# Kernel optimization log

Measured on AMD Instinct MI355X. Metric: run time of the kernel, lower is better.

## Reference

```python
import math
import jax, jax.numpy as jnp
import numpy as np

K_MODES = 8
L_ITERS = 8
ALPHA_INIT = 2000.0
TAU_INIT = 0.01


def setup_inputs() -> dict:
    key = jax.random.key(0)
    B, T, C = 64, 4096, 16
    x = jax.random.normal(key, (B, T, C), dtype=jnp.float32)
    log_alpha = jnp.full((L_ITERS, K_MODES), math.log(ALPHA_INIT), dtype=jnp.float32)
    raw_tau = jnp.full((L_ITERS,), math.log(math.expm1(TAU_INIT) + 1e-08), dtype=jnp.float32)
    omega_init = np.linspace(0.05, 0.45, K_MODES)
    raw_omega = jnp.asarray(np.log(2.0 * omega_init / (1.0 - 2.0 * omega_init + 1e-08)), dtype=jnp.float32)
    return {"x": x, "log_alpha": log_alpha, "raw_tau": raw_tau, "raw_omega": raw_omega}


def reference(x, log_alpha, raw_tau, raw_omega):
    B, T, C = x.shape
    L, K = log_alpha.shape
    T_rfft = T // 2 + 1

    alpha = jnp.exp(log_alpha)                    # (L, K)
    tau = jax.nn.softplus(raw_tau)                # (L,)
    omega = jax.nn.sigmoid(raw_omega) * 0.5       # (K,)

    freqs = jnp.linspace(0.0, 0.5, T_rfft, dtype=x.dtype)  # (T_rfft,)
    # (B, T, C) -> (B*C, T)
    x_bc = jnp.transpose(x, (0, 2, 1)).reshape(B * C, T)
    f_hat = jnp.fft.rfft(x_bc, axis=-1)           # (B*C, T_rfft) complex

    # Precompute all denominators: (L, K, T_rfft)
    denom = 1.0 + 2.0 * alpha[:, :, None] * (freqs[None, None, :] - omega[None, :, None]) ** 2

    u0 = jnp.zeros((B * C, K, T_rfft), dtype=f_hat.dtype)
    lam0 = jnp.zeros_like(f_hat)

    def step(carry, per_layer):
        u, lam = carry
        den_l, tau_l = per_layer
        u_sum = u.sum(axis=1)  # (B*C, T_rfft)
        # Jacobi update for all K modes simultaneously
        numerator = f_hat[:, None, :] - (u_sum[:, None, :] - u) + 0.5 * lam[:, None, :]
        u_new = numerator / den_l[None, :, :]
        lam_new = lam + tau_l * (f_hat - u_new.sum(axis=1))
        return (u_new, lam_new), None

    (u_final, _), _ = jax.lax.scan(step, (u0, lam0), (denom, tau))

    modes_flat = jnp.fft.irfft(u_final, n=T, axis=-1)  # (B*C, K, T)
    modes = jnp.transpose(modes_flat.reshape(B, C, K, T), (0, 2, 3, 1))  # (B, K, T, C)
    return modes
```

## Files before the change

kernel.cpp:

```cpp
#include <hip/hip_runtime.h>
#include <math.h>

#ifndef M_PI
#define M_PI 3.14159265358979323846
#endif

#define T_LEN 4096
#define M_LEN 2048
#define NFREQ 2049
#define KM 8
#define LI 8
#define CD 16

template <int NT>
__device__ __forceinline__ float2* fft2048(float2* a, float2* b, int tid, float sign) {
    float2* src = a;
    float2* dst = b;
    int l = 1024;
    #pragma unroll 1
    for (int s = 0; s < 11; ++s) {
        float piol = sign * (float)M_PI / (float)l;
        #pragma unroll
        for (int ii = 0; ii < 1024 / NT; ++ii) {
            int i = tid + ii * NT;
            int j = i >> s;
            float2 A = src[i];
            float2 B = src[i + 1024];
            float ang = piol * (float)j;
            float sw, cw;
            __sincosf(ang, &sw, &cw);
            float2 sum = make_float2(A.x + B.x, A.y + B.y);
            float2 dif = make_float2(A.x - B.x, A.y - B.y);
            float2 tw = make_float2(dif.x * cw - dif.y * sw, dif.x * sw + dif.y * cw);
            int p = i + (j << s);
            dst[p] = sum;
            dst[p + (1 << s)] = tw;
        }
        __syncthreads();
        float2* t = src; src = dst; dst = t;
        l >>= 1;
    }
    return src;
}

__global__ void __launch_bounds__(512)
k_fwd_iter(const float* __restrict__ x,
           const float* __restrict__ log_alpha,
           const float* __restrict__ raw_tau,
           const float* __restrict__ raw_omega,
           float2* __restrict__ u_ws)
{
    __shared__ float2 bufA[M_LEN];
    __shared__ float2 bufB[M_LEN];
    __shared__ float s_2a[LI * KM];
    __shared__ float s_tau[LI];
    __shared__ float s_om[KM];

    const int tid = threadIdx.x;
    const int row = blockIdx.x;
    const int b = row >> 4;
    const int c = row & 15;

    if (tid < LI * KM) s_2a[tid] = 2.0f * __expf(log_alpha[tid]);
    if (tid < LI)      s_tau[tid] = log1pf(__expf(raw_tau[tid]));
    if (tid < KM)      s_om[tid]  = 0.5f / (1.0f + __expf(-raw_omega[tid]));

    const float* xr = x + (size_t)b * T_LEN * CD + c;
    #pragma unroll
    for (int q = 0; q < 4; ++q) {
        int n = tid + q * 512;
        float e = xr[(size_t)(2 * n) * CD];
        float o = xr[(size_t)(2 * n + 1) * CD];
        bufA[n] = make_float2(e, o);
    }
    __syncthreads();

    float2* Z = fft2048<512>(bufA, bufB, tid, -1.0f);

    const size_t sb = (size_t)(b * (KM * CD) + c);

    for (int f = tid; f < NFREQ; f += 512) {
        float2 Zk = Z[f & (M_LEN - 1)];
        float2 Zm = Z[(M_LEN - f) & (M_LEN - 1)];
        float2 E = make_float2(0.5f * (Zk.x + Zm.x), 0.5f * (Zk.y - Zm.y));
        float2 D = make_float2(0.5f * (Zk.x - Zm.x), 0.5f * (Zk.y + Zm.y));
        float2 O = make_float2(D.y, -D.x);
        float ang = -2.0f * (float)M_PI * (float)f / (float)T_LEN;
        float sw, cw;
        __sincosf(ang, &sw, &cw);
        float fhx = E.x + cw * O.x - sw * O.y;
        float fhy = E.y + cw * O.y + sw * O.x;

        float freq = (float)f * (0.5f / (float)M_LEN);
        float dd[KM];
        #pragma unroll
        for (int k = 0; k < KM; ++k) {
            float d = freq - s_om[k];
            dd[k] = d * d;
        }

        float2 u[KM];
        #pragma unroll
        for (int k = 0; k < KM; ++k) u[k] = make_float2(0.f, 0.f);
        float lamx = 0.f, lamy = 0.f;

        #pragma unroll
        for (int l = 0; l < LI; ++l) {
            float usx = 0.f, usy = 0.f;
            #pragma unroll
            for (int k = 0; k < KM; ++k) { usx += u[k].x; usy += u[k].y; }
            float bx = fhx - usx + 0.5f * lamx;
            float by = fhy - usy + 0.5f * lamy;
            float sx = 0.f, sy = 0.f;
            #pragma unroll
            for (int k = 0; k < KM; ++k) {
                float den = fmaf(s_2a[l * KM + k], dd[k], 1.0f);
                float r = __builtin_amdgcn_rcpf(den);
                float ux = (bx + u[k].x) * r;
                float uy = (by + u[k].y) * r;
                u[k].x = ux; u[k].y = uy;
                sx += ux; sy += uy;
            }
            lamx += s_tau[l] * (fhx - sx);
            lamy += s_tau[l] * (fhy - sy);
        }

        #pragma unroll
        for (int k = 0; k < KM; ++k) {
            u_ws[(sb + (size_t)k * CD) * NFREQ + f] = u[k];
        }
    }
}

__global__ void __launch_bounds__(1024)
k_inv(const float2* __restrict__ u_ws, float* __restrict__ out)
{
    __shared__ float2 bufA[NFREQ];
    __shared__ float2 bufB[M_LEN];
    const int tid = threadIdx.x;
    const int bk = blockIdx.x;

    float val[CD][4];

    #pragma unroll
    for (int c = 0; c < CD; ++c) {
        const float2* sp = u_ws + (size_t)(bk * CD + c) * NFREQ;
        bufA[tid] = sp[tid];
        bufA[tid + 1024] = sp[tid + 1024];
        if (tid == 0) bufA[2048] = sp[2048];
        __syncthreads();

        #pragma unroll
        for (int jj = 0; jj < 2; ++jj) {
            int j = tid + jj * 1024;
            float2 Xj = bufA[j];
            float2 Xm = bufA[M_LEN - j];
            float2 E = make_float2(0.5f * (Xj.x + Xm.x), 0.5f * (Xj.y - Xm.y));
            float2 D = make_float2(0.5f * (Xj.x - Xm.x), 0.5f * (Xj.y + Xm.y));
            float ang = 2.0f * (float)M_PI * (float)j / (float)T_LEN;
            float sw, cw;
            __sincosf(ang, &sw, &cw);
            float2 O = make_float2(cw * D.x - sw * D.y, cw * D.y + sw * D.x);
            const float sc = 1.0f / (float)M_LEN;
            bufB[j] = make_float2((E.x - O.y) * sc, (E.y + O.x) * sc);
        }
        __syncthreads();

        float2* res = fft2048<1024>(bufB, bufA, tid, 1.0f);
        float2 z0 = res[2 * tid];
        float2 z1 = res[2 * tid + 1];
        val[c][0] = z0.x;
        val[c][1] = z0.y;
        val[c][2] = z1.x;
        val[c][3] = z1.y;
        __syncthreads();
    }

    float4* op = (float4*)(out + ((size_t)bk * T_LEN + (size_t)(4 * tid)) * CD);
    #pragma unroll
    for (int r = 0; r < 4; ++r) {
        #pragma unroll
        for (int g = 0; g < 4; ++g) {
            op[r * 4 + g] = make_float4(val[4 * g + 0][r], val[4 * g + 1][r],
                                        val[4 * g + 2][r], val[4 * g + 3][r]);
        }
    }
}

extern "C" void kernel_launch(void* const* d_in, const int* in_sizes, int n_in,
                              void* d_out, int out_size, void* d_ws, size_t ws_size,
                              hipStream_t stream) {
    const float* x         = (const float*)d_in[0];
    const float* log_alpha = (const float*)d_in[1];
    const float* raw_tau   = (const float*)d_in[2];
    const float* raw_omega = (const float*)d_in[3];
    float* out = (float*)d_out;
    float2* u_ws = (float2*)d_ws;

    k_fwd_iter<<<dim3(64 * CD), dim3(512), 0, stream>>>(x, log_alpha, raw_tau,
                                                        raw_omega, u_ws);
    k_inv<<<dim3(64 * KM), dim3(1024), 0, stream>>>(u_ws, out);
}
```

Measured before the change: 396.8 us.

## Process two channels per inverse-FFT pass and load spectrum directly from global

Measured after the change: 374.3 us. 1.06x faster.

```diff
diff --git a/kernel.cpp b/kernel.cpp
--- a/kernel.cpp
+++ b/kernel.cpp
@@ -135,45 +135,89 @@
 __global__ void __launch_bounds__(1024)
 k_inv(const float2* __restrict__ u_ws, float* __restrict__ out)
 {
-    __shared__ float2 bufA[NFREQ];
-    __shared__ float2 bufB[M_LEN];
+    __shared__ __align__(16) float2 buf[2][2][M_LEN];
+
     const int tid = threadIdx.x;
     const int bk = blockIdx.x;
 
     float val[CD][4];
-
-    #pragma unroll
-    for (int c = 0; c < CD; ++c) {
-        const float2* sp = u_ws + (size_t)(bk * CD + c) * NFREQ;
-        bufA[tid] = sp[tid];
-        bufA[tid + 1024] = sp[tid + 1024];
-        if (tid == 0) bufA[2048] = sp[2048];
-        __syncthreads();
-
-        #pragma unroll
-        for (int jj = 0; jj < 2; ++jj) {
-            int j = tid + jj * 1024;
-            float2 Xj = bufA[j];
-            float2 Xm = bufA[M_LEN - j];
-            float2 E = make_float2(0.5f * (Xj.x + Xm.x), 0.5f * (Xj.y - Xm.y));
-            float2 D = make_float2(0.5f * (Xj.x - Xm.x), 0.5f * (Xj.y + Xm.y));
-            float ang = 2.0f * (float)M_PI * (float)j / (float)T_LEN;
+    const float sc = 1.0f / (float)M_LEN;
+
+    #pragma unroll 1
+    for (int cp = 0; cp < 8; ++cp) {
+        if (cp > 0) {
+            #pragma unroll
+            for (int ch = 0; ch < 2; ++ch) {
+                int c = 2 * (cp - 1) + ch;
+                float4 z = *(const float4*)&buf[ch][1][2 * tid];
+                val[c][0] = z.x; val[c][1] = z.y; val[c][2] = z.z; val[c][3] = z.w;
+            }
+        }
+
+        #pragma unroll
+        for (int ch = 0; ch < 2; ++ch) {
+            int c = 2 * cp + ch;
+            const float2* sp = u_ws + (size_t)(bk * CD + c) * NFREQ;
+            int j = tid;
+            float2 Xj = sp[j];
+            float2 Xm = sp[M_LEN - j];
+            float Ex = 0.5f * (Xj.x + Xm.x), Ey = 0.5f * (Xj.y - Xm.y);
+            float Dx = 0.5f * (Xj.x - Xm.x), Dy = 0.5f * (Xj.y + Xm.y);
+            float ang = (2.0f * (float)M_PI / (float)T_LEN) * (float)j;
             float sw, cw;
             __sincosf(ang, &sw, &cw);
-            float2 O = make_float2(cw * D.x - sw * D.y, cw * D.y + sw * D.x);
-            const float sc = 1.0f / (float)M_LEN;
-            bufB[j] = make_float2((E.x - O.y) * sc, (E.y + O.x) * sc);
+            float Ox = cw * Dx - sw * Dy;
+            float Oy = cw * Dy + sw * Dx;
+            buf[ch][0][j] = make_float2((Ex - Oy) * sc, (Ey + Ox) * sc);
+            if (j > 0) {
+                buf[ch][0][M_LEN - j] = make_float2((Ex + Oy) * sc, (Ox - Ey) * sc);
+            } else {
+                float2 Xq = sp[1024];
+                buf[ch][0][1024] = make_float2(Xq.x * sc, -Xq.y * sc);
+            }
         }
         __syncthreads();
 
-        float2* res = fft2048<1024>(bufB, bufA, tid, 1.0f);
-        float2 z0 = res[2 * tid];
-        float2 z1 = res[2 * tid + 1];
-        val[c][0] = z0.x;
-        val[c][1] = z0.y;
-        val[c][2] = z1.x;
-        val[c][3] = z1.y;
-        __syncthreads();
+        float2* s0 = buf[0][0]; float2* d0 = buf[0][1];
+        float2* s1 = buf[1][0]; float2* d1 = buf[1][1];
+        #pragma unroll 1
+        for (int s = 0; s < 11; ++s) {
+            const int i = tid;
+            const int j = i >> s;
+            const int m = 1 << s;
+            const int p = i + (j << s);
+            float ang = ((float)M_PI / 1024.0f) * (float)(j << s);
+            float sw, cw;
+            __sincosf(ang, &sw, &cw);
+            {
+                float2 A = s0[i], B = s0[i + 1024];
+                float2 sum = make_float2(A.x + B.x, A.y + B.y);
+                float2 dif = make_float2(A.x - B.x, A.y - B.y);
+                float2 t = make_float2(dif.x * cw - dif.y * sw,
+                                       dif.x * sw + dif.y * cw);
+                d0[p] = sum;
+                d0[p + m] = t;
+            }
+            {
+                float2 A = s1[i], B = s1[i + 1024];
+                float2 sum = make_float2(A.x + B.x, A.y + B.y);
+                float2 dif = make_float2(A.x - B.x, A.y - B.y);
+                float2 t = make_float2(dif.x * cw - dif.y * sw,
+                                       dif.x * sw + dif.y * cw);
+                d1[p] = sum;
+                d1[p + m] = t;
+            }
+            __syncthreads();
+            float2* t0 = s0; s0 = d0; d0 = t0;
+            float2* t1 = s1; s1 = d1; d1 = t1;
+        }
+    }
+
+    #pragma unroll
+    for (int ch = 0; ch < 2; ++ch) {
+        int c = 14 + ch;
+        float4 z = *(const float4*)&buf[ch][1][2 * tid];
+        val[c][0] = z.x; val[c][1] = z.y; val[c][2] = z.z; val[c][3] = z.w;
     }
 
     float4* op = (float4*)(out + ((size_t)bk * T_LEN + (size_t)(4 * tid)) * CD);
```

## Rewrite inverse FFT as in-place radix-8 Stockham with four channels per block

Applied to the files above, without the earlier changes.

New measurement: 414.8 us. +4.5%, slower.

```diff
diff --git a/kernel.cpp b/kernel.cpp
--- a/kernel.cpp
+++ b/kernel.cpp
@@ -11,6 +11,71 @@
 #define KM 8
 #define LI 8
 #define CD 16
+
+__device__ __forceinline__ float2 cadd(float2 a, float2 b){ return make_float2(a.x+b.x, a.y+b.y); }
+__device__ __forceinline__ float2 csub(float2 a, float2 b){ return make_float2(a.x-b.x, a.y-b.y); }
+__device__ __forceinline__ float2 cmul(float2 a, float2 b){ return make_float2(a.x*b.x - a.y*b.y, a.x*b.y + a.y*b.x); }
+__device__ __forceinline__ float2 muli(float2 a){ return make_float2(-a.y, a.x); }
+#define RC 0.70710678118654752440f
+__device__ __forceinline__ float2 mulw81(float2 a){ return make_float2(RC*(a.x-a.y), RC*(a.x+a.y)); }
+__device__ __forceinline__ float2 mulw83(float2 a){ return make_float2(-RC*(a.x+a.y), RC*(a.x-a.y)); }
+
+#define SWZ(i) ((i) ^ (((i) >> 4) & 15))
+
+__device__ __forceinline__ void dft8_inv(const float2 a[8], float2 x[8]) {
+    float2 s0=cadd(a[0],a[4]), s1=cadd(a[1],a[5]), s2=cadd(a[2],a[6]), s3=cadd(a[3],a[7]);
+    float2 d0=csub(a[0],a[4]), d1=csub(a[1],a[5]), d2=csub(a[2],a[6]), d3=csub(a[3],a[7]);
+    d1 = mulw81(d1); d2 = muli(d2); d3 = mulw83(d3);
+    float2 e0=cadd(s0,s2), e2=csub(s0,s2), e1=cadd(s1,s3), e3=muli(csub(s1,s3));
+    float2 f0=cadd(d0,d2), f2=csub(d0,d2), f1=cadd(d1,d3), f3=muli(csub(d1,d3));
+    x[0]=cadd(e0,e1); x[4]=csub(e0,e1); x[2]=cadd(e2,e3); x[6]=csub(e2,e3);
+    x[1]=cadd(f0,f1); x[5]=csub(f0,f1); x[3]=cadd(f2,f3); x[7]=csub(f2,f3);
+}
+
+template<int MSTAGE>
+__device__ __forceinline__ void r8_stage(float2* S, int lt) {
+    float2 a[8];
+    #pragma unroll
+    for (int k = 0; k < 8; ++k) a[k] = S[SWZ(lt + 256*k)];
+    __syncthreads();
+    float2 x[8];
+    dft8_inv(a, x);
+    const int j = lt / MSTAGE;
+    const int r = lt % MSTAGE;
+    float th = ((float)M_PI / 1024.0f) * (float)(j * MSTAGE);
+    float swv, cwv; __sincosf(th, &swv, &cwv);
+    float2 w1 = make_float2(cwv, swv);
+    float2 w2 = cmul(w1,w1), w3 = cmul(w2,w1), w4 = cmul(w2,w2);
+    float2 w5 = cmul(w3,w2), w6 = cmul(w3,w3), w7 = cmul(w4,w3);
+    x[1]=cmul(x[1],w1); x[2]=cmul(x[2],w2); x[3]=cmul(x[3],w3);
+    x[4]=cmul(x[4],w4); x[5]=cmul(x[5],w5); x[6]=cmul(x[6],w6); x[7]=cmul(x[7],w7);
+    const int base = r + 8*MSTAGE*j;
+    #pragma unroll
+    for (int k = 0; k < 8; ++k) S[SWZ(base + MSTAGE*k)] = x[k];
+    __syncthreads();
+}
+
+__device__ __forceinline__ void r4_stage_pair(float2* S, int lt) {
+    float2 b[2][4];
+    #pragma unroll
+    for (int h = 0; h < 2; ++h) {
+        int i2 = lt + 256*h;
+        #pragma unroll
+        for (int k = 0; k < 4; ++k) b[h][k] = S[SWZ(i2 + 512*k)];
+    }
+    __syncthreads();
+    #pragma unroll
+    for (int h = 0; h < 2; ++h) {
+        int i2 = lt + 256*h;
+        float2 s02=cadd(b[h][0],b[h][2]), d02=csub(b[h][0],b[h][2]);
+        float2 s13=cadd(b[h][1],b[h][3]), d13=muli(csub(b[h][1],b[h][3]));
+        S[SWZ(i2 +    0)] = cadd(s02,s13);
+        S[SWZ(i2 +  512)] = cadd(d02,d13);
+        S[SWZ(i2 + 1024)] = csub(s02,s13);
+        S[SWZ(i2 + 1536)] = csub(d02,d13);
+    }
+    __syncthreads();
+}
 
 template <int NT>
 __device__ __forceinline__ float2* fft2048(float2* a, float2* b, int tid, float sign) {
@@ -135,54 +200,67 @@
 __global__ void __launch_bounds__(1024)
 k_inv(const float2* __restrict__ u_ws, float* __restrict__ out)
 {
-    __shared__ float2 bufA[NFREQ];
-    __shared__ float2 bufB[M_LEN];
+    __shared__ float2 S[4][M_LEN];
+
     const int tid = threadIdx.x;
-    const int bk = blockIdx.x;
+    const int g   = tid >> 8;
+    const int lt  = tid & 255;
+    const int bk  = blockIdx.x;
 
     float val[CD][4];
-
-    #pragma unroll
-    for (int c = 0; c < CD; ++c) {
-        const float2* sp = u_ws + (size_t)(bk * CD + c) * NFREQ;
-        bufA[tid] = sp[tid];
-        bufA[tid + 1024] = sp[tid + 1024];
-        if (tid == 0) bufA[2048] = sp[2048];
+    const float sc = 1.0f / (float)M_LEN;
+
+    #pragma unroll
+    for (int cp = 0; cp < 4; ++cp) {
+        const int c0 = 4 * cp;
+        const float2* sp = u_ws + (size_t)(bk * CD + c0 + g) * NFREQ;
+
+        #pragma unroll
+        for (int q = 0; q < 4; ++q) {
+            int j = lt + 256 * q;
+            float2 Xj = sp[j];
+            float2 Xm = sp[M_LEN - j];
+            float Ex = 0.5f * (Xj.x + Xm.x), Ey = 0.5f * (Xj.y - Xm.y);
+            float Dx = 0.5f * (Xj.x - Xm.x), Dy = 0.5f * (Xj.y + Xm.y);
+            float ang = (2.0f * (float)M_PI / (float)T_LEN) * (float)j;
+            float swv, cwv;
+            __sincosf(ang, &swv, &cwv);
+            float Ox = cwv * Dx - swv * Dy;
+            float Oy = cwv * Dy + swv * Dx;
+            S[g][SWZ(j)] = make_float2((Ex - Oy) * sc, (Ey + Ox) * sc);
+            if (j > 0) {
+                S[g][SWZ(M_LEN - j)] = make_float2((Ex + Oy) * sc, (Ox - Ey) * sc);
+            } else {
+                float2 Xq = sp[1024];
+                S[g][SWZ(1024)] = make_float2(Xq.x * sc, -Xq.y * sc);
+            }
+        }
         __syncthreads();
 
-        #pragma unroll
-        for (int jj = 0; jj < 2; ++jj) {
-            int j = tid + jj * 1024;
-            float2 Xj = bufA[j];
-            float2 Xm = bufA[M_LEN - j];
-            float2 E = make_float2(0.5f * (Xj.x + Xm.x), 0.5f * (Xj.y - Xm.y));
-            float2 D = make_float2(0.5f * (Xj.x - Xm.x), 0.5f * (Xj.y + Xm.y));
-            float ang = 2.0f * (float)M_PI * (float)j / (float)T_LEN;
-            float sw, cw;
-            __sincosf(ang, &sw, &cw);
-            float2 O = make_float2(cw * D.x - sw * D.y, cw * D.y + sw * D.x);
-            const float sc = 1.0f / (float)M_LEN;
-            bufB[j] = make_float2((E.x - O.y) * sc, (E.y + O.x) * sc);
+        r8_stage<1>(S[g], lt);
+        r8_stage<8>(S[g], lt);
+        r8_stage<64>(S[g], lt);
+        r4_stage_pair(S[g], lt);
+
+        #pragma unroll
+        for (int cc = 0; cc < 4; ++cc) {
+            float2 z0 = S[cc][SWZ(2 * tid)];
+            float2 z1 = S[cc][SWZ(2 * tid + 1)];
+            val[c0 + cc][0] = z0.x;
+            val[c0 + cc][1] = z0.y;
+            val[c0 + cc][2] = z1.x;
+            val[c0 + cc][3] = z1.y;
         }
         __syncthreads();
-
-        float2* res = fft2048<1024>(bufB, bufA, tid, 1.0f);
-        float2 z0 = res[2 * tid];
-        float2 z1 = res[2 * tid + 1];
-        val[c][0] = z0.x;
-        val[c][1] = z0.y;
-        val[c][2] = z1.x;
-        val[c][3] = z1.y;
-        __syncthreads();
     }
 
     float4* op = (float4*)(out + ((size_t)bk * T_LEN + (size_t)(4 * tid)) * CD);
     #pragma unroll
     for (int r = 0; r < 4; ++r) {
         #pragma unroll
-        for (int g = 0; g < 4; ++g) {
-            op[r * 4 + g] = make_float4(val[4 * g + 0][r], val[4 * g + 1][r],
-                                        val[4 * g + 2][r], val[4 * g + 3][r]);
+        for (int g2 = 0; g2 < 4; ++g2) {
+            op[r * 4 + g2] = make_float4(val[4 * g2 + 0][r], val[4 * g2 + 1][r],
+                                         val[4 * g2 + 2][r], val[4 * g2 + 3][r]);
         }
     }
 }
```

## Use radix-8 in-place FFT with swizzled LDS in forward kernel, two rows per block

Applied to the files above, without the earlier changes.

New measurement: 393.9 us. Within noise of the previous version (-0.7%).

```diff
diff --git a/kernel.cpp b/kernel.cpp
--- a/kernel.cpp
+++ b/kernel.cpp
@@ -11,6 +11,88 @@
 #define KM 8
 #define LI 8
 #define CD 16
+
+__device__ __forceinline__ float2 cadd(float2 a, float2 b){ return make_float2(a.x+b.x, a.y+b.y); }
+__device__ __forceinline__ float2 csub(float2 a, float2 b){ return make_float2(a.x-b.x, a.y-b.y); }
+__device__ __forceinline__ float2 cmul(float2 a, float2 b){ return make_float2(a.x*b.x - a.y*b.y, a.x*b.y + a.y*b.x); }
+#define RC 0.70710678118654752440f
+
+template<int SGN>
+__device__ __forceinline__ float2 muli_s(float2 a){
+    return (SGN > 0) ? make_float2(-a.y, a.x) : make_float2(a.y, -a.x);
+}
+template<int SGN>
+__device__ __forceinline__ float2 w81_s(float2 a){
+    return (SGN > 0) ? make_float2(RC*(a.x-a.y), RC*(a.x+a.y))
+                     : make_float2(RC*(a.x+a.y), RC*(a.y-a.x));
+}
+template<int SGN>
+__device__ __forceinline__ float2 w83_s(float2 a){
+    return (SGN > 0) ? make_float2(-RC*(a.x+a.y), RC*(a.x-a.y))
+                     : make_float2(RC*(a.y-a.x), -RC*(a.x+a.y));
+}
+
+#define SWZ(i) ((i) ^ (((i) >> 4) & 15))
+
+template<int SGN>
+__device__ __forceinline__ void dft8_s(const float2 a[8], float2 x[8]) {
+    float2 s0=cadd(a[0],a[4]), s1=cadd(a[1],a[5]), s2=cadd(a[2],a[6]), s3=cadd(a[3],a[7]);
+    float2 d0=csub(a[0],a[4]), d1=csub(a[1],a[5]), d2=csub(a[2],a[6]), d3=csub(a[3],a[7]);
+    d1 = w81_s<SGN>(d1); d2 = muli_s<SGN>(d2); d3 = w83_s<SGN>(d3);
+    float2 e0=cadd(s0,s2), e2=csub(s0,s2), e1=cadd(s1,s3), e3=muli_s<SGN>(csub(s1,s3));
+    float2 f0=cadd(d0,d2), f2=csub(d0,d2), f1=cadd(d1,d3), f3=muli_s<SGN>(csub(d1,d3));
+    x[0]=cadd(e0,e1); x[4]=csub(e0,e1); x[2]=cadd(e2,e3); x[6]=csub(e2,e3);
+    x[1]=cadd(f0,f1); x[5]=csub(f0,f1); x[3]=cadd(f2,f3); x[7]=csub(f2,f3);
+}
+
+template<int MSTAGE, int SGN>
+__device__ __forceinline__ void r8_stage(float2* S, int lt) {
+    float2 a[8];
+    #pragma unroll
+    for (int k = 0; k < 8; ++k) a[k] = S[SWZ(lt + 256*k)];
+    __syncthreads();
+    float2 x[8];
+    dft8_s<SGN>(a, x);
+    const int j = lt / MSTAGE;
+    const int r = lt % MSTAGE;
+    float th = (float)SGN * ((float)M_PI / 1024.0f) * (float)(j * MSTAGE);
+    float swv, cwv; __sincosf(th, &swv, &cwv);
+    const float2 w1 = make_float2(cwv, swv);
+    float2 w = w1;
+    x[1] = cmul(x[1], w);
+    #pragma unroll
+    for (int k = 2; k < 8; ++k) {
+        w = cmul(w, w1);
+        x[k] = cmul(x[k], w);
+    }
+    const int base = r + 8*MSTAGE*j;
+    #pragma unroll
+    for (int k = 0; k < 8; ++k) S[SWZ(base + MSTAGE*k)] = x[k];
+    __syncthreads();
+}
+
+template<int SGN>
+__device__ __forceinline__ void r4_stage_pair(float2* S, int lt) {
+    float2 b[2][4];
+    #pragma unroll
+    for (int h = 0; h < 2; ++h) {
+        int i2 = lt + 256*h;
+        #pragma unroll
+        for (int k = 0; k < 4; ++k) b[h][k] = S[SWZ(i2 + 512*k)];
+    }
+    __syncthreads();
+    #pragma unroll
+    for (int h = 0; h < 2; ++h) {
+        int i2 = lt + 256*h;
+        float2 s02=cadd(b[h][0],b[h][2]), d02=csub(b[h][0],b[h][2]);
+        float2 s13=cadd(b[h][1],b[h][3]), d13=muli_s<SGN>(csub(b[h][1],b[h][3]));
+        S[SWZ(i2 +    0)] = cadd(s02,s13);
+        S[SWZ(i2 +  512)] = cadd(d02,d13);
+        S[SWZ(i2 + 1024)] = csub(s02,s13);
+        S[SWZ(i2 + 1536)] = csub(d02,d13);
+    }
+    __syncthreads();
+}
 
 template <int NT>
 __device__ __forceinline__ float2* fft2048(float2* a, float2* b, int tid, float sign) {
@@ -50,38 +132,42 @@
            const float* __restrict__ raw_omega,
            float2* __restrict__ u_ws)
 {
-    __shared__ float2 bufA[M_LEN];
-    __shared__ float2 bufB[M_LEN];
+    __shared__ float2 S[2][M_LEN];
     __shared__ float s_2a[LI * KM];
-    __shared__ float s_tau[LI];
+    __shared__ float s_tau2[LI];
     __shared__ float s_om[KM];
 
     const int tid = threadIdx.x;
-    const int row = blockIdx.x;
+    const int g   = tid >> 8;
+    const int lt  = tid & 255;
+    const int row = blockIdx.x * 2 + g;
     const int b = row >> 4;
     const int c = row & 15;
 
-    if (tid < LI * KM) s_2a[tid] = 2.0f * __expf(log_alpha[tid]);
-    if (tid < LI)      s_tau[tid] = log1pf(__expf(raw_tau[tid]));
+    if (tid < LI * KM) s_2a[tid]  = 2.0f * __expf(log_alpha[tid]);
+    if (tid < LI)      s_tau2[tid] = 0.5f * log1pf(__expf(raw_tau[tid]));
     if (tid < KM)      s_om[tid]  = 0.5f / (1.0f + __expf(-raw_omega[tid]));
 
     const float* xr = x + (size_t)b * T_LEN * CD + c;
     #pragma unroll
-    for (int q = 0; q < 4; ++q) {
-        int n = tid + q * 512;
+    for (int q = 0; q < 8; ++q) {
+        int n = lt + 256 * q;
         float e = xr[(size_t)(2 * n) * CD];
         float o = xr[(size_t)(2 * n + 1) * CD];
-        bufA[n] = make_float2(e, o);
-    }
-    __syncthreads();
-
-    float2* Z = fft2048<512>(bufA, bufB, tid, -1.0f);
+        S[g][SWZ(n)] = make_float2(e, o);
+    }
+    __syncthreads();
+
+    r8_stage<1,  -1>(S[g], lt);
+    r8_stage<8,  -1>(S[g], lt);
+    r8_stage<64, -1>(S[g], lt);
+    r4_stage_pair<-1>(S[g], lt);
 
     const size_t sb = (size_t)(b * (KM * CD) + c);
 
-    for (int f = tid; f < NFREQ; f += 512) {
-        float2 Zk = Z[f & (M_LEN - 1)];
-        float2 Zm = Z[(M_LEN - f) & (M_LEN - 1)];
+    for (int f = lt; f < NFREQ; f += 256) {
+        float2 Zk = S[g][SWZ(f & (M_LEN - 1))];
+        float2 Zm = S[g][SWZ((M_LEN - f) & (M_LEN - 1))];
         float2 E = make_float2(0.5f * (Zk.x + Zm.x), 0.5f * (Zk.y - Zm.y));
         float2 D = make_float2(0.5f * (Zk.x - Zm.x), 0.5f * (Zk.y + Zm.y));
         float2 O = make_float2(D.y, -D.x);
@@ -100,18 +186,30 @@
         }
 
         float2 u[KM];
-        #pragma unroll
-        for (int k = 0; k < KM; ++k) u[k] = make_float2(0.f, 0.f);
-        float lamx = 0.f, lamy = 0.f;
-
-        #pragma unroll
-        for (int l = 0; l < LI; ++l) {
-            float usx = 0.f, usy = 0.f;
+        float sx, sy;
+        float hx = 0.f, hy = 0.f;
+
+        {
+            float nsx = 0.f, nsy = 0.f;
             #pragma unroll
-            for (int k = 0; k < KM; ++k) { usx += u[k].x; usy += u[k].y; }
-            float bx = fhx - usx + 0.5f * lamx;
-            float by = fhy - usy + 0.5f * lamy;
-            float sx = 0.f, sy = 0.f;
+            for (int k = 0; k < KM; ++k) {
+                float den = fmaf(s_2a[k], dd[k], 1.0f);
+                float r = __builtin_amdgcn_rcpf(den);
+                float ux = fhx * r;
+                float uy = fhy * r;
+                u[k].x = ux; u[k].y = uy;
+                nsx += ux; nsy += uy;
+            }
+            hx = s_tau2[0] * (fhx - nsx);
+            hy = s_tau2[0] * (fhy - nsy);
+            sx = nsx; sy = nsy;
+        }
+
+        #pragma unroll
+        for (int l = 1; l < LI; ++l) {
+            float bx = fhx - sx + hx;
+            float by = fhy - sy + hy;
+            float nsx = 0.f, nsy = 0.f;
             #pragma unroll
             for (int k = 0; k < KM; ++k) {
                 float den = fmaf(s_2a[l * KM + k], dd[k], 1.0f);
@@ -119,10 +217,11 @@
                 float ux = (bx + u[k].x) * r;
                 float uy = (by + u[k].y) * r;
                 u[k].x = ux; u[k].y = uy;
-                sx += ux; sy += uy;
+                nsx += ux; nsy += uy;
             }
-            lamx += s_tau[l] * (fhx - sx);
-            lamy += s_tau[l] * (fhy - sy);
+            hx += s_tau2[l] * (fhx - nsx);
+            hy += s_tau2[l] * (fhy - nsy);
+            sx = nsx; sy = nsy;
         }
 
         #pragma unroll
@@ -197,7 +296,7 @@
     float* out = (float*)d_out;
     float2* u_ws = (float2*)d_ws;
 
-    k_fwd_iter<<<dim3(64 * CD), dim3(512), 0, stream>>>(x, log_alpha, raw_tau,
-                                                        raw_omega, u_ws);
+    k_fwd_iter<<<dim3(64 * CD / 2), dim3(512), 0, stream>>>(x, log_alpha, raw_tau,
+                                                            raw_omega, u_ws);
     k_inv<<<dim3(64 * KM), dim3(1024), 0, stream>>>(u_ws, out);
 }
```
